# Optimization experiments

Hardware: AMD Instinct MI355X
Metric: run time of the kernel (lower is better)

Reference implementation:

```python
import jax, jax.numpy as jnp
import numpy as np
from jax import lax

NB = 65536          # voxels (seeds) per batch element
C = 256             # feature dim
NUM_CLASS = 3
MAX_NPOINTS = 4096  # per-batch top-k keep
FPS_NPOINTS = 2048  # farthest-point samples
OFFSET_RANGE = np.array([3.0, 3.0, 2.0], dtype=np.float32)
BN_EPS = 1e-5


def _bn_relu(x, gamma, beta):
    # nn.BatchNorm1d in training mode: batch statistics over N
    m = jnp.mean(x, axis=0)
    v = jnp.var(x, axis=0)
    return jax.nn.relu((x - m) * lax.rsqrt(v + BN_EPS) * gamma + beta)


def _vote_mlp(x, w1, g1, b1, w2, b2):
    # Linear(bias=False) -> BN -> ReLU -> Linear(bias)
    return _bn_relu(x @ w1, g1, b1) @ w2 + b2


def _fps(xyz, k):
    # D-FPS (PointNet++ furthest_point_sample): start at index 0,
    # iteratively pick the point with max min-distance to selected set.
    M = xyz.shape[0]

    def step(carry, _):
        dist, last = carry
        d = jnp.sum((xyz - xyz[last]) ** 2, axis=-1)
        dist = jnp.minimum(dist, d)
        nxt = jnp.argmax(dist).astype(jnp.int32)
        return (dist, nxt), nxt

    init = (jnp.full((M,), 1e10, xyz.dtype), jnp.int32(0))
    _, idxs = lax.scan(step, init, None, length=k - 1)
    return jnp.concatenate([jnp.zeros((1,), jnp.int32), idxs])


def setup_inputs() -> dict:
    key = jax.random.key(0)
    ks = jax.random.split(key, 8)
    B = 4
    N = B * NB
    seed_xyz = jax.random.uniform(ks[0], (N, 3), jnp.float32) * jnp.array([70.0, 80.0, 4.0]) - jnp.array([0.0, 40.0, 3.0])
    seed_feats = jax.random.normal(ks[1], (N, C), jnp.float32)
    s = 0.02
    inp = {
        "seed_xyz": seed_xyz,
        "seed_feats": seed_feats,
        "w_off1": jax.random.normal(ks[2], (C, C), jnp.float32) * s,
        "g_off1": jnp.ones((C,), jnp.float32),
        "be_off1": jnp.zeros((C,), jnp.float32),
        "w_off2": jax.random.normal(ks[3], (C, 3), jnp.float32) * s,
        "b_off2": jnp.zeros((3,), jnp.float32),
        "w_cls1": jax.random.normal(ks[4], (C, C), jnp.float32) * s,
        "g_cls1": jnp.ones((C,), jnp.float32),
        "be_cls1": jnp.zeros((C,), jnp.float32),
        "w_cls2": jax.random.normal(ks[5], (C, NUM_CLASS), jnp.float32) * s,
        "b_cls2": jnp.full((NUM_CLASS,), -2.19, jnp.float32),  # cls bias init fill(-2.19)
        "batch_size": B,
    }
    return inp


def reference(seed_xyz, seed_feats, w_off1, g_off1, be_off1, w_off2, b_off2,
              w_cls1, g_cls1, be_cls1, w_cls2, b_cls2, batch_size):
    B = int(batch_size)
    off_rng = jnp.asarray(OFFSET_RANGE)

    # VoteLayer
    seed_offset = _vote_mlp(seed_feats, w_off1, g_off1, be_off1, w_off2, b_off2)   # (N,3)
    seed_cls = _vote_mlp(seed_feats, w_cls1, g_cls1, be_cls1, w_cls2, b_cls2)      # (N,num_class)
    limited = jnp.clip(seed_offset, -off_rng, off_rng)
    votes_xyz = seed_xyz + limited                                                 # (N,3)

    # fps_pool_layer: per-batch topk + D-FPS
    scores = jnp.max(seed_cls, axis=-1)                                            # (N,)
    scores_b = scores.reshape(B, NB)
    xyz_b = seed_xyz.reshape(B, NB, 3)

    def per_batch(sc, xyz):
        _, topk_idx = lax.top_k(jax.nn.sigmoid(sc), MAX_NPOINTS)   # (K,)
        fidx = _fps(xyz[topk_idx], FPS_NPOINTS)                    # (P,) local in topk set
        return topk_idx[fidx]                                      # remap to per-batch index

    local_idx = jax.vmap(per_batch)(scores_b, xyz_b)               # (B, P)
    fps_indices = (local_idx + jnp.arange(B, dtype=local_idx.dtype)[:, None] * NB).reshape(-1)

    bs_col = jnp.repeat(jnp.arange(B, dtype=jnp.float32), NB)[:, None]
    seeds = jnp.concatenate([bs_col, seed_xyz], axis=-1)           # (N,4)
    votes = jnp.concatenate([bs_col, votes_xyz], axis=-1)          # (N,4)

    vote_candidates = lax.stop_gradient(votes[fps_indices])        # .detach() in torch
    vote_features = seed_feats[fps_indices]                        # (B*P, C)

    return (vote_candidates, vote_features, seeds, seed_cls, votes, fps_indices)
```

## Files before the change

kernel.cpp:

```cpp
#include <hip/hip_runtime.h>

#define NB_V 65536
#define TOPK 4096
#define FPSK 2048

typedef short bf16x8 __attribute__((ext_vector_type(8)));
typedef float f32x4 __attribute__((ext_vector_type(4)));

__global__ __launch_bounds__(256, 2) void k_gemm_bf(const float* __restrict__ A,
                                                    const float* __restrict__ W,
                                                    float* __restrict__ H, int N) {
  __shared__ unsigned short As[64][264];
  __shared__ unsigned short Bs[64][264];
  const int tid = threadIdx.x;
  const int cb = blockIdx.x & 3;
  const int rb = blockIdx.x >> 2;
#pragma unroll
  for (int l = 0; l < 16; ++l) {
    int f = tid + 256 * l;
    int r = f >> 6, c4 = (f & 63) << 2;
    float4 v = *reinterpret_cast<const float4*>(&A[(size_t)(rb * 64 + r) * 256 + c4]);
    ushort4 u;
    u.x = (unsigned short)(__float_as_uint(v.x) >> 16);
    u.y = (unsigned short)(__float_as_uint(v.y) >> 16);
    u.z = (unsigned short)(__float_as_uint(v.z) >> 16);
    u.w = (unsigned short)(__float_as_uint(v.w) >> 16);
    *reinterpret_cast<ushort4*>(&As[r][c4]) = u;
  }
  {
    const int c = tid & 63;
    const int kg = tid >> 6;
#pragma unroll
    for (int j = 0; j < 16; ++j) {
      int k0 = kg * 64 + j * 4;
      ushort4 u;
      u.x = (unsigned short)(__float_as_uint(W[(size_t)(k0 + 0) * 256 + cb * 64 + c]) >> 16);
      u.y = (unsigned short)(__float_as_uint(W[(size_t)(k0 + 1) * 256 + cb * 64 + c]) >> 16);
      u.z = (unsigned short)(__float_as_uint(W[(size_t)(k0 + 2) * 256 + cb * 64 + c]) >> 16);
      u.w = (unsigned short)(__float_as_uint(W[(size_t)(k0 + 3) * 256 + cb * 64 + c]) >> 16);
      *reinterpret_cast<ushort4*>(&Bs[c][k0]) = u;
    }
  }
  __syncthreads();
  const int lane = tid & 63, w = tid >> 6;
  const int m = lane & 15, kq = lane >> 4;
  f32x4 acc[4];
#pragma unroll
  for (int s = 0; s < 4; ++s) acc[s] = (f32x4){0.f, 0.f, 0.f, 0.f};
#pragma unroll
  for (int k0 = 0; k0 < 256; k0 += 32) {
    bf16x8 a = *reinterpret_cast<const bf16x8*>(&As[w * 16 + m][k0 + kq * 8]);
#pragma unroll
    for (int s = 0; s < 4; ++s) {
      bf16x8 bfr = *reinterpret_cast<const bf16x8*>(&Bs[s * 16 + m][k0 + kq * 8]);
      acc[s] = __builtin_amdgcn_mfma_f32_16x16x32_bf16(a, bfr, acc[s], 0, 0, 0);
    }
  }
#pragma unroll
  for (int s = 0; s < 4; ++s)
#pragma unroll
    for (int i = 0; i < 4; ++i)
      H[(size_t)(rb * 64 + w * 16 + kq * 4 + i) * 256 + cb * 64 + s * 16 + m] = acc[s][i];
}

__global__ __launch_bounds__(256) void k_gemm64(const float* __restrict__ A,
                                                const float* __restrict__ W,
                                                float* __restrict__ H, int N) {
  __shared__ double Asm[64][33];
  __shared__ double Bsm[32][65];
  const int tid = threadIdx.x;
  const int tx = tid & 15, ty = tid >> 4;
  const int cb = blockIdx.x & 3;
  const int rb = blockIdx.x >> 2;
  double acc[4][4];
#pragma unroll
  for (int i = 0; i < 4; ++i)
#pragma unroll
    for (int j = 0; j < 4; ++j) acc[i][j] = 0.0;

  for (int kc = 0; kc < 256; kc += 32) {
#pragma unroll
    for (int l = 0; l < 8; ++l) {
      int f = tid + 256 * l;
      int r = f >> 5, c = f & 31;
      Asm[r][c] = (double)A[(size_t)(rb * 64 + r) * 256 + kc + c];
    }
#pragma unroll
    for (int l = 0; l < 8; ++l) {
      int f = tid + 256 * l;
      int kr = f >> 6, c = f & 63;
      Bsm[kr][c] = (double)W[(size_t)(kc + kr) * 256 + cb * 64 + c];
    }
    __syncthreads();
#pragma unroll 4
    for (int kk = 0; kk < 32; ++kk) {
      double a0[4], b0[4];
#pragma unroll
      for (int i = 0; i < 4; ++i) a0[i] = Asm[ty + 16 * i][kk];
#pragma unroll
      for (int j = 0; j < 4; ++j) b0[j] = Bsm[kk][tx + 16 * j];
#pragma unroll
      for (int i = 0; i < 4; ++i)
#pragma unroll
        for (int j = 0; j < 4; ++j) acc[i][j] += a0[i] * b0[j];
    }
    __syncthreads();
  }
#pragma unroll
  for (int i = 0; i < 4; ++i)
#pragma unroll
    for (int j = 0; j < 4; ++j)
      H[(size_t)(rb * 64 + ty + 16 * i) * 256 + cb * 64 + tx + 16 * j] = (float)acc[i][j];
}

__global__ __launch_bounds__(256) void k_stats(const float* __restrict__ Hoff,
                                               const float* __restrict__ Hcls,
                                               double* __restrict__ part, int N) {
  const int rpb = N / 1024;
  const int r0 = blockIdx.x * rpb;
  const int t = threadIdx.x;
  double s0 = 0, q0 = 0, s1 = 0, q1 = 0;
  for (int r = r0; r < r0 + rpb; ++r) {
    double v = (double)Hoff[(size_t)r * 256 + t];
    s0 += v; q0 = fma(v, v, q0);
    double w = (double)Hcls[(size_t)r * 256 + t];
    s1 += w; q1 = fma(w, w, q1);
  }
  double* o = part + ((size_t)blockIdx.x * 512 + t) * 2;
  o[0] = s0; o[1] = q0;
  o = part + ((size_t)blockIdx.x * 512 + 256 + t) * 2;
  o[0] = s1; o[1] = q1;
}

__global__ void k_statsfin(const double* __restrict__ part,
                           const float* __restrict__ g_off, const float* __restrict__ be_off,
                           const float* __restrict__ g_cls, const float* __restrict__ be_cls,
                           double* __restrict__ aarr, double* __restrict__ carr,
                           int nparts, int N) {
  const int c = threadIdx.x;
  double s = 0, q = 0;
  for (int p = 0; p < nparts; ++p) {
    s += part[((size_t)p * 512 + c) * 2];
    q += part[((size_t)p * 512 + c) * 2 + 1];
  }
  double mean = s / (double)N;
  double var = q / (double)N - mean * mean;
  double g = (c < 256) ? (double)g_off[c] : (double)g_cls[c - 256];
  double be = (c < 256) ? (double)be_off[c] : (double)be_cls[c - 256];
  double a = g / sqrt(var + 1e-5);
  aarr[c] = a;
  carr[c] = be - mean * a;
}

__global__ __launch_bounds__(256) void k_fuse(const float* __restrict__ Hoff,
                                              const float* __restrict__ Hcls,
                                              const float* __restrict__ xyz,
                                              const float* __restrict__ w_off2,
                                              const float* __restrict__ b_off2,
                                              const float* __restrict__ w_cls2,
                                              const float* __restrict__ b_cls2,
                                              const double* __restrict__ aarr,
                                              const double* __restrict__ carr,
                                              float* __restrict__ out_seeds,
                                              float* __restrict__ out_cls,
                                              float* __restrict__ out_votes,
                                              unsigned long long* __restrict__ keys,
                                              int N) {
  __shared__ double sa[512], sc[512];
  __shared__ double w2[512][3];
  const int tid = threadIdx.x;
  for (int i = tid; i < 512; i += 256) {
    sa[i] = aarr[i];
    sc[i] = carr[i];
#pragma unroll
    for (int k = 0; k < 3; ++k)
      w2[i][k] = (i < 256) ? (double)w_off2[i * 3 + k] : (double)w_cls2[(i - 256) * 3 + k];
  }
  __syncthreads();
  const int lane = tid & 63, wid = tid >> 6;
  const int gw = blockIdx.x * 4 + wid;
  for (int r = gw; r < N; r += 4096) {
    double po0 = 0, po1 = 0, po2 = 0, pc0 = 0, pc1 = 0, pc2 = 0;
#pragma unroll
    for (int q = 0; q < 4; ++q) {
      int c = lane + 64 * q;
      double h = (double)Hoff[(size_t)r * 256 + c];
      double v = fma(h, sa[c], sc[c]);
      v = v > 0.0 ? v : 0.0;
      po0 = fma(v, w2[c][0], po0);
      po1 = fma(v, w2[c][1], po1);
      po2 = fma(v, w2[c][2], po2);
      int c2 = 256 + c;
      double h2 = (double)Hcls[(size_t)r * 256 + c];
      double v2 = fma(h2, sa[c2], sc[c2]);
      v2 = v2 > 0.0 ? v2 : 0.0;
      pc0 = fma(v2, w2[c2][0], pc0);
      pc1 = fma(v2, w2[c2][1], pc1);
      pc2 = fma(v2, w2[c2][2], pc2);
    }
#pragma unroll
    for (int off = 32; off; off >>= 1) {
      po0 += __shfl_xor(po0, off); po1 += __shfl_xor(po1, off); po2 += __shfl_xor(po2, off);
      pc0 += __shfl_xor(pc0, off); pc1 += __shfl_xor(pc1, off); pc2 += __shfl_xor(pc2, off);
    }
    if (lane == 0) {
      float x = xyz[(size_t)r * 3], y = xyz[(size_t)r * 3 + 1], z = xyz[(size_t)r * 3 + 2];
      float bs = (float)(r >> 16);
      out_seeds[(size_t)r * 4 + 0] = bs;
      out_seeds[(size_t)r * 4 + 1] = x;
      out_seeds[(size_t)r * 4 + 2] = y;
      out_seeds[(size_t)r * 4 + 3] = z;
      double offv[3] = {po0 + (double)b_off2[0], po1 + (double)b_off2[1], po2 + (double)b_off2[2]};
      const double rng[3] = {3.0, 3.0, 2.0};
      float pxyz[3] = {x, y, z};
      out_votes[(size_t)r * 4 + 0] = bs;
#pragma unroll
      for (int k = 0; k < 3; ++k) {
        double lim = offv[k];
        lim = lim < -rng[k] ? -rng[k] : lim;
        lim = lim > rng[k] ? rng[k] : lim;
        out_votes[(size_t)r * 4 + 1 + k] = (float)((double)pxyz[k] + lim);
      }
      double c0 = pc0 + (double)b_cls2[0];
      double c1 = pc1 + (double)b_cls2[1];
      double c2v = pc2 + (double)b_cls2[2];
      out_cls[(size_t)r * 3 + 0] = (float)c0;
      out_cls[(size_t)r * 3 + 1] = (float)c1;
      out_cls[(size_t)r * 3 + 2] = (float)c2v;
      double s = c0 > c1 ? c0 : c1;
      s = s > c2v ? s : c2v;
      long long bits = __double_as_longlong(s);
      unsigned long long key =
          bits >= 0 ? ((unsigned long long)bits | 0x8000000000000000ull) : ~((unsigned long long)bits);
      keys[r] = key;
    }
  }
}

__global__ __launch_bounds__(1024) void k_topk(const unsigned long long* __restrict__ keys,
                                               unsigned int* __restrict__ topk) {
  const int b = blockIdx.x;
  const unsigned long long* K = keys + (size_t)b * NB_V;
  __shared__ unsigned int hist[256];
  __shared__ unsigned long long pfx_s;
  __shared__ int want_s;
  __shared__ unsigned long long skey[TOPK];
  __shared__ unsigned int sidx[TOPK];
  __shared__ int cnt_hi, cnt_eq;
  __shared__ unsigned int eq_idx[1024];
  const int tid = threadIdx.x;
  if (tid == 0) { pfx_s = 0ull; want_s = TOPK; }
  __syncthreads();
  for (int p = 0; p < 8; ++p) {
    const int shift = 56 - 8 * p;
    if (tid < 256) hist[tid] = 0;
    __syncthreads();
    unsigned long long pfx = pfx_s;
    for (int i = tid; i < NB_V; i += 1024) {
      unsigned long long k = K[i];
      bool ok;
      if (p == 0) ok = true;
      else ok = ((k >> (shift + 8)) == (pfx >> (shift + 8)));
      if (ok) atomicAdd(&hist[(unsigned)(k >> shift) & 255u], 1u);
    }
    __syncthreads();
    if (tid == 0) {
      int want = want_s;
      int cum = 0, d = 255;
      for (; d >= 0; --d) {
        int c = (int)hist[d];
        if (cum + c >= want) break;
        cum += c;
      }
      want_s = want - cum;
      pfx_s = pfx_s | ((unsigned long long)d << shift);
    }
    __syncthreads();
  }
  const unsigned long long Kthr = pfx_s;
  const int T = want_s;
  if (tid == 0) { cnt_hi = 0; cnt_eq = 0; }
  __syncthreads();
  for (int i = tid; i < NB_V; i += 1024) {
    unsigned long long k = K[i];
    if (k > Kthr) {
      int pos = atomicAdd(&cnt_hi, 1);
      skey[pos] = k;
      sidx[pos] = (unsigned)i;
    } else if (k == Kthr) {
      int pos = atomicAdd(&cnt_eq, 1);
      if (pos < 1024) eq_idx[pos] = (unsigned)i;
    }
  }
  __syncthreads();
  if (tid == 0) {
    int m = cnt_eq; if (m > 1024) m = 1024;
    for (int a2 = 1; a2 < m; ++a2) {
      unsigned v = eq_idx[a2];
      int b2 = a2 - 1;
      while (b2 >= 0 && eq_idx[b2] > v) { eq_idx[b2 + 1] = eq_idx[b2]; --b2; }
      eq_idx[b2 + 1] = v;
    }
    for (int t = 0; t < T; ++t) { skey[cnt_hi + t] = Kthr; sidx[cnt_hi + t] = eq_idx[t]; }
  }
  __syncthreads();
  for (int k2 = 2; k2 <= TOPK; k2 <<= 1) {
    for (int j = k2 >> 1; j > 0; j >>= 1) {
      for (int i = tid; i < TOPK; i += 1024) {
        int ix = i ^ j;
        if (ix > i) {
          unsigned long long ka = skey[i], kb = skey[ix];
          unsigned int ia = sidx[i], ib = sidx[ix];
          bool a_first = (ka > kb) || (ka == kb && ia < ib);
          bool up = (i & k2) == 0;
          if (up ? !a_first : a_first) {
            skey[i] = kb; skey[ix] = ka;
            sidx[i] = ib; sidx[ix] = ia;
          }
        }
      }
      __syncthreads();
    }
  }
  for (int i = tid; i < TOPK; i += 1024) topk[(size_t)b * TOPK + i] = sidx[i];
}

template <int CTRL>
__device__ __forceinline__ void dpp_merge2(unsigned long long& v, int& p) {
  unsigned lo = (unsigned)v, hi = (unsigned)(v >> 32);
  unsigned olo = (unsigned)__builtin_amdgcn_update_dpp(0, (int)lo, CTRL, 0xF, 0xF, false);
  unsigned ohi = (unsigned)__builtin_amdgcn_update_dpp(0, (int)hi, CTRL, 0xF, 0xF, false);
  int op = __builtin_amdgcn_update_dpp(0, p, CTRL, 0xF, 0xF, false);
  unsigned long long ov = ((unsigned long long)ohi << 32) | (unsigned long long)olo;
  bool t = (ov > v) || (ov == v && op < p);
  v = t ? ov : v;
  p = t ? op : p;
}

__device__ __forceinline__ void shfl_merge2(unsigned long long& v, int& p, int mask) {
  unsigned long long ov = __shfl_xor(v, mask);
  int op = __shfl_xor(p, mask);
  bool t = (ov > v) || (ov == v && op < p);
  v = t ? ov : v;
  p = t ? op : p;
}

#define FPS_REP16(M) M(0) M(1) M(2) M(3) M(4) M(5) M(6) M(7) \
                     M(8) M(9) M(10) M(11) M(12) M(13) M(14) M(15)

__global__ __launch_bounds__(256, 1) void k_fps(const float* __restrict__ xyz,
                                                const unsigned int* __restrict__ topk,
                                                unsigned int* __restrict__ fpspos) {
  const int b = blockIdx.x;
  const int tid = threadIdx.x;
  __shared__ float4 cpos[TOPK];
  __shared__ ulonglong2 wv[2][4];
  __shared__ float4 wc[2][4];

#define FPS_DECL(J) float x##J, y##J, z##J; double d##J;
  FPS_REP16(FPS_DECL)

#define FPS_INIT(J) { \
    int p = tid + 256 * (J); \
    unsigned idx = topk[(size_t)b * TOPK + p]; \
    size_t base = ((size_t)b * NB_V + idx) * 3; \
    x##J = xyz[base]; y##J = xyz[base + 1]; z##J = xyz[base + 2]; \
    d##J = 1e10; \
    cpos[p] = make_float4(x##J, y##J, z##J, 0.0f); }
  FPS_REP16(FPS_INIT)

  if (tid == 0) {
    wc[0][0] = make_float4(x0, y0, z0, 0.0f);
    fpspos[(size_t)b * FPSK] = 0u;
  }
  __syncthreads();
  float4 s0 = wc[0][0];
  float sx = s0.x, sy = s0.y, sz = s0.z;
  const int lane = tid & 63, wid = tid >> 6;

  for (int it = 1; it < FPSK; ++it) {
    const int par = it & 1;
    double lx = (double)sx, ly = (double)sy, lz = (double)sz;
    unsigned long long cv0, cv1;
    int cp0, cp1;
#define FPS_UPD(J) { \
    double dx = (double)x##J - lx; \
    double dy = (double)y##J - ly; \
    double dz = (double)z##J - lz; \
    double dd = __dadd_rn(__dadd_rn(__dmul_rn(dx, dx), __dmul_rn(dy, dy)), __dmul_rn(dz, dz)); \
    d##J = fmin(d##J, dd); \
    unsigned long long db = (unsigned long long)__double_as_longlong(d##J); \
    if ((J) == 0) { cv0 = db; cp0 = tid; } \
    else if ((J) == 1) { cv1 = db; cp1 = tid + 256; } \
    else if (((J) & 1) == 0) { bool g = db > cv0; cv0 = g ? db : cv0; cp0 = g ? (tid + 256 * (J)) : cp0; } \
    else { bool g = db > cv1; cv1 = g ? db : cv1; cp1 = g ? (tid + 256 * (J)) : cp1; } }
    FPS_REP16(FPS_UPD)
    {
      bool g = (cv1 > cv0) || (cv1 == cv0 && cp1 < cp0);
      cv0 = g ? cv1 : cv0;
      cp0 = g ? cp1 : cp0;
    }
    dpp_merge2<0xB1>(cv0, cp0);
    dpp_merge2<0x4E>(cv0, cp0);
    dpp_merge2<0x124>(cv0, cp0);
    dpp_merge2<0x128>(cv0, cp0);
    shfl_merge2(cv0, cp0, 16);
    shfl_merge2(cv0, cp0, 32);
    float4 wpos = cpos[cp0];
    if (lane == 0) {
      wv[par][wid] = make_ulonglong2(cv0, (unsigned long long)(unsigned)cp0);
      wc[par][wid] = wpos;
    }
    __syncthreads();
    ulonglong2 e0 = wv[par][0];
    float4 q0 = wc[par][0];
    unsigned long long bv = e0.x;
    int bp = (int)e0.y;
    float fx = q0.x, fy = q0.y, fz = q0.z;
#pragma unroll
    for (int w = 1; w < 4; ++w) {
      ulonglong2 e = wv[par][w];
      float4 q = wc[par][w];
      bool t = (e.x > bv) || (e.x == bv && (int)e.y < bp);
      bv = t ? e.x : bv;
      bp = t ? (int)e.y : bp;
      fx = t ? q.x : fx;
      fy = t ? q.y : fy;
      fz = t ? q.z : fz;
    }
    sx = fx; sy = fy; sz = fz;
    if (tid == 0) fpspos[(size_t)b * FPSK + it] = (unsigned)bp;
  }
}

__global__ __launch_bounds__(256) void k_gather(const unsigned int* __restrict__ topk,
                                                const unsigned int* __restrict__ fpspos,
                                                const float* __restrict__ feats,
                                                const float* __restrict__ votes_out,
                                                float* __restrict__ o0, float* __restrict__ o1,
                                                float* __restrict__ o5) {
  const int r = blockIdx.x;
  const int b = r / FPSK;
  __shared__ unsigned int gsh;
  if (threadIdx.x == 0) {
    unsigned pos = fpspos[r];
    unsigned local = topk[(size_t)b * TOPK + pos];
    gsh = (unsigned)(b * NB_V) + local;
  }
  __syncthreads();
  const unsigned g = gsh;
  o1[(size_t)r * 256 + threadIdx.x] = feats[(size_t)g * 256 + threadIdx.x];
  if (threadIdx.x < 4) o0[(size_t)r * 4 + threadIdx.x] = votes_out[(size_t)g * 4 + threadIdx.x];
  if (threadIdx.x == 4) o5[r] = (float)g;
}

extern "C" void kernel_launch(void* const* d_in, const int* in_sizes, int n_in,
                              void* d_out, int out_size, void* d_ws, size_t ws_size,
                              hipStream_t stream) {
  const float* xyz = (const float*)d_in[0];
  const float* feats = (const float*)d_in[1];
  const float* w_off1 = (const float*)d_in[2];
  const float* g_off1 = (const float*)d_in[3];
  const float* be_off1 = (const float*)d_in[4];
  const float* w_off2 = (const float*)d_in[5];
  const float* b_off2 = (const float*)d_in[6];
  const float* w_cls1 = (const float*)d_in[7];
  const float* g_cls1 = (const float*)d_in[8];
  const float* be_cls1 = (const float*)d_in[9];
  const float* w_cls2 = (const float*)d_in[10];
  const float* b_cls2 = (const float*)d_in[11];

  const int N = in_sizes[0] / 3;
  const int B = N / NB_V;
  const int BP = B * FPSK;

  float* out = (float*)d_out;
  float* o0 = out;
  float* o1 = o0 + (size_t)BP * 4;
  float* o2 = o1 + (size_t)BP * 256;
  float* o3 = o2 + (size_t)N * 4;
  float* o4 = o3 + (size_t)N * 3;
  float* o5 = o4 + (size_t)N * 4;

  char* w = (char*)d_ws;
  float* Hoff = (float*)w;
  float* Hcls = (float*)(w + (size_t)N * 1024);
  double* part = (double*)(w + (size_t)N * 2048);
  double* aarr = (double*)(w + (size_t)N * 2048 + 8388608);
  double* carr = aarr + 512;
  unsigned long long* keys =
      (unsigned long long*)(w + (size_t)N * 2048 + 8388608 + 8192);
  unsigned int* topkbuf = (unsigned int*)((char*)keys + (size_t)N * 8);
  unsigned int* fpspos = topkbuf + (size_t)B * TOPK;

  k_gemm_bf<<<dim3((N / 64) * 4), dim3(256), 0, stream>>>(feats, w_off1, Hoff, N);
  k_gemm64<<<dim3((N / 64) * 4), dim3(256), 0, stream>>>(feats, w_cls1, Hcls, N);
  k_stats<<<dim3(1024), dim3(256), 0, stream>>>(Hoff, Hcls, part, N);
  k_statsfin<<<dim3(1), dim3(512), 0, stream>>>(part, g_off1, be_off1, g_cls1, be_cls1,
                                                aarr, carr, 1024, N);
  k_fuse<<<dim3(1024), dim3(256), 0, stream>>>(Hoff, Hcls, xyz, w_off2, b_off2, w_cls2,
                                               b_cls2, aarr, carr, o2, o3, o4, keys, N);
  k_topk<<<dim3(B), dim3(1024), 0, stream>>>(keys, topkbuf);
  k_fps<<<dim3(B), dim3(256), 0, stream>>>(xyz, topkbuf, fpspos);
  k_gather<<<dim3(BP), dim3(256), 0, stream>>>(topkbuf, fpspos, feats, o4, o0, o1, o5);
}
```

Measured before the change: 4.160 ms.

## Overlap serial FPS with offset-branch GEMM by reordering pipeline and fusing kernels

```diff
diff --git a/kernel.cpp b/kernel.cpp
--- a/kernel.cpp
+++ b/kernel.cpp
@@ -6,62 +6,6 @@
 
 typedef short bf16x8 __attribute__((ext_vector_type(8)));
 typedef float f32x4 __attribute__((ext_vector_type(4)));
-
-__global__ __launch_bounds__(256, 2) void k_gemm_bf(const float* __restrict__ A,
-                                                    const float* __restrict__ W,
-                                                    float* __restrict__ H, int N) {
-  __shared__ unsigned short As[64][264];
-  __shared__ unsigned short Bs[64][264];
-  const int tid = threadIdx.x;
-  const int cb = blockIdx.x & 3;
-  const int rb = blockIdx.x >> 2;
-#pragma unroll
-  for (int l = 0; l < 16; ++l) {
-    int f = tid + 256 * l;
-    int r = f >> 6, c4 = (f & 63) << 2;
-    float4 v = *reinterpret_cast<const float4*>(&A[(size_t)(rb * 64 + r) * 256 + c4]);
-    ushort4 u;
-    u.x = (unsigned short)(__float_as_uint(v.x) >> 16);
-    u.y = (unsigned short)(__float_as_uint(v.y) >> 16);
-    u.z = (unsigned short)(__float_as_uint(v.z) >> 16);
-    u.w = (unsigned short)(__float_as_uint(v.w) >> 16);
-    *reinterpret_cast<ushort4*>(&As[r][c4]) = u;
-  }
-  {
-    const int c = tid & 63;
-    const int kg = tid >> 6;
-#pragma unroll
-    for (int j = 0; j < 16; ++j) {
-      int k0 = kg * 64 + j * 4;
-      ushort4 u;
-      u.x = (unsigned short)(__float_as_uint(W[(size_t)(k0 + 0) * 256 + cb * 64 + c]) >> 16);
-      u.y = (unsigned short)(__float_as_uint(W[(size_t)(k0 + 1) * 256 + cb * 64 + c]) >> 16);
-      u.z = (unsigned short)(__float_as_uint(W[(size_t)(k0 + 2) * 256 + cb * 64 + c]) >> 16);
-      u.w = (unsigned short)(__float_as_uint(W[(size_t)(k0 + 3) * 256 + cb * 64 + c]) >> 16);
-      *reinterpret_cast<ushort4*>(&Bs[c][k0]) = u;
-    }
-  }
-  __syncthreads();
-  const int lane = tid & 63, w = tid >> 6;
-  const int m = lane & 15, kq = lane >> 4;
-  f32x4 acc[4];
-#pragma unroll
-  for (int s = 0; s < 4; ++s) acc[s] = (f32x4){0.f, 0.f, 0.f, 0.f};
-#pragma unroll
-  for (int k0 = 0; k0 < 256; k0 += 32) {
-    bf16x8 a = *reinterpret_cast<const bf16x8*>(&As[w * 16 + m][k0 + kq * 8]);
-#pragma unroll
-    for (int s = 0; s < 4; ++s) {
-      bf16x8 bfr = *reinterpret_cast<const bf16x8*>(&Bs[s * 16 + m][k0 + kq * 8]);
-      acc[s] = __builtin_amdgcn_mfma_f32_16x16x32_bf16(a, bfr, acc[s], 0, 0, 0);
-    }
-  }
-#pragma unroll
-  for (int s = 0; s < 4; ++s)
-#pragma unroll
-    for (int i = 0; i < 4; ++i)
-      H[(size_t)(rb * 64 + w * 16 + kq * 4 + i) * 256 + cb * 64 + s * 16 + m] = acc[s][i];
-}
 
 __global__ __launch_bounds__(256) void k_gemm64(const float* __restrict__ A,
                                                 const float* __restrict__ W,
@@ -113,95 +57,78 @@
       H[(size_t)(rb * 64 + ty + 16 * i) * 256 + cb * 64 + tx + 16 * j] = (float)acc[i][j];
 }
 
-__global__ __launch_bounds__(256) void k_stats(const float* __restrict__ Hoff,
-                                               const float* __restrict__ Hcls,
-                                               double* __restrict__ part, int N) {
+__global__ __launch_bounds__(256) void k_stats1(const float* __restrict__ H,
+                                                double* __restrict__ part, int N) {
   const int rpb = N / 1024;
   const int r0 = blockIdx.x * rpb;
   const int t = threadIdx.x;
-  double s0 = 0, q0 = 0, s1 = 0, q1 = 0;
+  double s = 0, q = 0;
   for (int r = r0; r < r0 + rpb; ++r) {
-    double v = (double)Hoff[(size_t)r * 256 + t];
-    s0 += v; q0 = fma(v, v, q0);
-    double w = (double)Hcls[(size_t)r * 256 + t];
-    s1 += w; q1 = fma(w, w, q1);
-  }
-  double* o = part + ((size_t)blockIdx.x * 512 + t) * 2;
-  o[0] = s0; o[1] = q0;
-  o = part + ((size_t)blockIdx.x * 512 + 256 + t) * 2;
-  o[0] = s1; o[1] = q1;
-}
-
-__global__ void k_statsfin(const double* __restrict__ part,
-                           const float* __restrict__ g_off, const float* __restrict__ be_off,
-                           const float* __restrict__ g_cls, const float* __restrict__ be_cls,
-                           double* __restrict__ aarr, double* __restrict__ carr,
-                           int nparts, int N) {
+    double v = (double)H[(size_t)r * 256 + t];
+    s += v;
+    q = fma(v, v, q);
+  }
+  double* o = part + ((size_t)blockIdx.x * 256 + t) * 2;
+  o[0] = s;
+  o[1] = q;
+}
+
+__global__ void k_statsfin1(const double* __restrict__ part,
+                            const float* __restrict__ gam, const float* __restrict__ bet,
+                            double* __restrict__ aarr, double* __restrict__ carr,
+                            int nparts, int N) {
   const int c = threadIdx.x;
   double s = 0, q = 0;
   for (int p = 0; p < nparts; ++p) {
-    s += part[((size_t)p * 512 + c) * 2];
-    q += part[((size_t)p * 512 + c) * 2 + 1];
+    s += part[((size_t)p * 256 + c) * 2];
+    q += part[((size_t)p * 256 + c) * 2 + 1];
   }
   double mean = s / (double)N;
   double var = q / (double)N - mean * mean;
-  double g = (c < 256) ? (double)g_off[c] : (double)g_cls[c - 256];
-  double be = (c < 256) ? (double)be_off[c] : (double)be_cls[c - 256];
-  double a = g / sqrt(var + 1e-5);
+  double a = (double)gam[c] / sqrt(var + 1e-5);
   aarr[c] = a;
-  carr[c] = be - mean * a;
-}
-
-__global__ __launch_bounds__(256) void k_fuse(const float* __restrict__ Hoff,
-                                              const float* __restrict__ Hcls,
-                                              const float* __restrict__ xyz,
-                                              const float* __restrict__ w_off2,
-                                              const float* __restrict__ b_off2,
-                                              const float* __restrict__ w_cls2,
-                                              const float* __restrict__ b_cls2,
-                                              const double* __restrict__ aarr,
-                                              const double* __restrict__ carr,
-                                              float* __restrict__ out_seeds,
-                                              float* __restrict__ out_cls,
-                                              float* __restrict__ out_votes,
-                                              unsigned long long* __restrict__ keys,
-                                              int N) {
-  __shared__ double sa[512], sc[512];
-  __shared__ double w2[512][3];
+  carr[c] = (double)bet[c] - mean * a;
+}
+
+__global__ __launch_bounds__(256) void k_fuse_cls(const float* __restrict__ Hcls,
+                                                  const float* __restrict__ xyz,
+                                                  const float* __restrict__ w_cls2,
+                                                  const float* __restrict__ b_cls2,
+                                                  const double* __restrict__ aarr,
+                                                  const double* __restrict__ carr,
+                                                  float* __restrict__ out_seeds,
+                                                  float* __restrict__ out_cls,
+                                                  unsigned long long* __restrict__ keys,
+                                                  int N) {
+  __shared__ double sa[256], sc[256];
+  __shared__ double w2[256][3];
   const int tid = threadIdx.x;
-  for (int i = tid; i < 512; i += 256) {
-    sa[i] = aarr[i];
-    sc[i] = carr[i];
-#pragma unroll
-    for (int k = 0; k < 3; ++k)
-      w2[i][k] = (i < 256) ? (double)w_off2[i * 3 + k] : (double)w_cls2[(i - 256) * 3 + k];
+  {
+    sa[tid] = aarr[tid];
+    sc[tid] = carr[tid];
+#pragma unroll
+    for (int k = 0; k < 3; ++k) w2[tid][k] = (double)w_cls2[tid * 3 + k];
   }
   __syncthreads();
   const int lane = tid & 63, wid = tid >> 6;
   const int gw = blockIdx.x * 4 + wid;
   for (int r = gw; r < N; r += 4096) {
-    double po0 = 0, po1 = 0, po2 = 0, pc0 = 0, pc1 = 0, pc2 = 0;
+    double pc0 = 0, pc1 = 0, pc2 = 0;
 #pragma unroll
     for (int q = 0; q < 4; ++q) {
       int c = lane + 64 * q;
-      double h = (double)Hoff[(size_t)r * 256 + c];
-      double v = fma(h, sa[c], sc[c]);
-      v = v > 0.0 ? v : 0.0;
-      po0 = fma(v, w2[c][0], po0);
-      po1 = fma(v, w2[c][1], po1);
-      po2 = fma(v, w2[c][2], po2);
-      int c2 = 256 + c;
       double h2 = (double)Hcls[(size_t)r * 256 + c];
-      double v2 = fma(h2, sa[c2], sc[c2]);
+      double v2 = fma(h2, sa[c], sc[c]);
       v2 = v2 > 0.0 ? v2 : 0.0;
-      pc0 = fma(v2, w2[c2][0], pc0);
-      pc1 = fma(v2, w2[c2][1], pc1);
-      pc2 = fma(v2, w2[c2][2], pc2);
+      pc0 = fma(v2, w2[c][0], pc0);
+      pc1 = fma(v2, w2[c][1], pc1);
+      pc2 = fma(v2, w2[c][2], pc2);
     }
 #pragma unroll
     for (int off = 32; off; off >>= 1) {
-      po0 += __shfl_xor(po0, off); po1 += __shfl_xor(po1, off); po2 += __shfl_xor(po2, off);
-      pc0 += __shfl_xor(pc0, off); pc1 += __shfl_xor(pc1, off); pc2 += __shfl_xor(pc2, off);
+      pc0 += __shfl_xor(pc0, off);
+      pc1 += __shfl_xor(pc1, off);
+      pc2 += __shfl_xor(pc2, off);
     }
     if (lane == 0) {
       float x = xyz[(size_t)r * 3], y = xyz[(size_t)r * 3 + 1], z = xyz[(size_t)r * 3 + 2];
@@ -210,17 +137,6 @@
       out_seeds[(size_t)r * 4 + 1] = x;
       out_seeds[(size_t)r * 4 + 2] = y;
       out_seeds[(size_t)r * 4 + 3] = z;
-      double offv[3] = {po0 + (double)b_off2[0], po1 + (double)b_off2[1], po2 + (double)b_off2[2]};
-      const double rng[3] = {3.0, 3.0, 2.0};
-      float pxyz[3] = {x, y, z};
-      out_votes[(size_t)r * 4 + 0] = bs;
-#pragma unroll
-      for (int k = 0; k < 3; ++k) {
-        double lim = offv[k];
-        lim = lim < -rng[k] ? -rng[k] : lim;
-        lim = lim > rng[k] ? rng[k] : lim;
-        out_votes[(size_t)r * 4 + 1 + k] = (float)((double)pxyz[k] + lim);
-      }
       double c0 = pc0 + (double)b_cls2[0];
       double c1 = pc1 + (double)b_cls2[1];
       double c2v = pc2 + (double)b_cls2[2];
@@ -233,6 +149,62 @@
       unsigned long long key =
           bits >= 0 ? ((unsigned long long)bits | 0x8000000000000000ull) : ~((unsigned long long)bits);
       keys[r] = key;
+    }
+  }
+}
+
+__global__ __launch_bounds__(256) void k_fuse_off(const float* __restrict__ Hoff,
+                                                  const float* __restrict__ xyz,
+                                                  const float* __restrict__ w_off2,
+                                                  const float* __restrict__ b_off2,
+                                                  const double* __restrict__ aarr,
+                                                  const double* __restrict__ carr,
+                                                  float* __restrict__ out_votes,
+                                                  int N) {
+  __shared__ double sa[256], sc[256];
+  __shared__ double w2[256][3];
+  const int tid = threadIdx.x;
+  {
+    sa[tid] = aarr[tid];
+    sc[tid] = carr[tid];
+#pragma unroll
+    for (int k = 0; k < 3; ++k) w2[tid][k] = (double)w_off2[tid * 3 + k];
+  }
+  __syncthreads();
+  const int lane = tid & 63, wid = tid >> 6;
+  const int gw = blockIdx.x * 4 + wid;
+  for (int r = gw; r < N; r += 4096) {
+    double po0 = 0, po1 = 0, po2 = 0;
+#pragma unroll
+    for (int q = 0; q < 4; ++q) {
+      int c = lane + 64 * q;
+      double h = (double)Hoff[(size_t)r * 256 + c];
+      double v = fma(h, sa[c], sc[c]);
+      v = v > 0.0 ? v : 0.0;
+      po0 = fma(v, w2[c][0], po0);
+      po1 = fma(v, w2[c][1], po1);
+      po2 = fma(v, w2[c][2], po2);
+    }
+#pragma unroll
+    for (int off = 32; off; off >>= 1) {
+      po0 += __shfl_xor(po0, off);
+      po1 += __shfl_xor(po1, off);
+      po2 += __shfl_xor(po2, off);
+    }
+    if (lane == 0) {
+      float x = xyz[(size_t)r * 3], y = xyz[(size_t)r * 3 + 1], z = xyz[(size_t)r * 3 + 2];
+      float bs = (float)(r >> 16);
+      double offv[3] = {po0 + (double)b_off2[0], po1 + (double)b_off2[1], po2 + (double)b_off2[2]};
+      const double rng[3] = {3.0, 3.0, 2.0};
+      float pxyz[3] = {x, y, z};
+      out_votes[(size_t)r * 4 + 0] = bs;
+#pragma unroll
+      for (int k = 0; k < 3; ++k) {
+        double lim = offv[k];
+        lim = lim < -rng[k] ? -rng[k] : lim;
+        lim = lim > rng[k] ? rng[k] : lim;
+        out_votes[(size_t)r * 4 + 1 + k] = (float)((double)pxyz[k] + lim);
+      }
     }
   }
 }
@@ -337,28 +309,32 @@
   p = t ? op : p;
 }
 
-__device__ __forceinline__ void shfl_merge2(unsigned long long& v, int& p, int mask) {
-  unsigned long long ov = __shfl_xor(v, mask);
-  int op = __shfl_xor(p, mask);
-  bool t = (ov > v) || (ov == v && op < p);
-  v = t ? ov : v;
-  p = t ? op : p;
+__device__ __forceinline__ unsigned long long rdlane64(unsigned long long v, int l) {
+  unsigned lo = (unsigned)__builtin_amdgcn_readlane((int)(unsigned)v, l);
+  unsigned hi = (unsigned)__builtin_amdgcn_readlane((int)(unsigned)(v >> 32), l);
+  return ((unsigned long long)hi << 32) | (unsigned long long)lo;
 }
 
 #define FPS_REP16(M) M(0) M(1) M(2) M(3) M(4) M(5) M(6) M(7) \
                      M(8) M(9) M(10) M(11) M(12) M(13) M(14) M(15)
 
-__global__ __launch_bounds__(256, 1) void k_fps(const float* __restrict__ xyz,
-                                                const unsigned int* __restrict__ topk,
-                                                unsigned int* __restrict__ fpspos) {
-  const int b = blockIdx.x;
+__global__ __launch_bounds__(256, 2) void k_fused(const float* __restrict__ xyz,
+                                                  const unsigned int* __restrict__ topk,
+                                                  unsigned int* __restrict__ fpspos,
+                                                  const float* __restrict__ A,
+                                                  const float* __restrict__ W,
+                                                  float* __restrict__ H, int N) {
+  __shared__ __align__(16) char smem[67584];
   const int tid = threadIdx.x;
-  __shared__ float4 cpos[TOPK];
-  __shared__ ulonglong2 wv[2][4];
-  __shared__ float4 wc[2][4];
+
+  if (blockIdx.x < 4) {
+    float4* cpos = (float4*)smem;
+    ulonglong2(*wv)[4] = (ulonglong2(*)[4])(smem + 65536);
+    float4(*wc)[4] = (float4(*)[4])(smem + 65792);
+    const int b = blockIdx.x;
 
 #define FPS_DECL(J) float x##J, y##J, z##J; double d##J;
-  FPS_REP16(FPS_DECL)
+    FPS_REP16(FPS_DECL)
 
 #define FPS_INIT(J) { \
     int p = tid + 256 * (J); \
@@ -367,22 +343,22 @@
     x##J = xyz[base]; y##J = xyz[base + 1]; z##J = xyz[base + 2]; \
     d##J = 1e10; \
     cpos[p] = make_float4(x##J, y##J, z##J, 0.0f); }
-  FPS_REP16(FPS_INIT)
-
-  if (tid == 0) {
-    wc[0][0] = make_float4(x0, y0, z0, 0.0f);
-    fpspos[(size_t)b * FPSK] = 0u;
-  }
-  __syncthreads();
-  float4 s0 = wc[0][0];
-  float sx = s0.x, sy = s0.y, sz = s0.z;
-  const int lane = tid & 63, wid = tid >> 6;
-
-  for (int it = 1; it < FPSK; ++it) {
-    const int par = it & 1;
-    double lx = (double)sx, ly = (double)sy, lz = (double)sz;
-    unsigned long long cv0, cv1;
-    int cp0, cp1;
+    FPS_REP16(FPS_INIT)
+
+    if (tid == 0) {
+      wc[0][0] = make_float4(x0, y0, z0, 0.0f);
+      fpspos[(size_t)b * FPSK] = 0u;
+    }
+    __syncthreads();
+    float4 s0 = wc[0][0];
+    float sx = s0.x, sy = s0.y, sz = s0.z;
+    const int lane = tid & 63, wid = tid >> 6;
+
+    for (int it = 1; it < FPSK; ++it) {
+      const int par = it & 1;
+      double lx = (double)sx, ly = (double)sy, lz = (double)sz;
+      unsigned long long cv0, cv1;
+      int cp0, cp1;
 #define FPS_UPD(J) { \
     double dx = (double)x##J - lx; \
     double dy = (double)y##J - ly; \
@@ -394,42 +370,102 @@
     else if ((J) == 1) { cv1 = db; cp1 = tid + 256; } \
     else if (((J) & 1) == 0) { bool g = db > cv0; cv0 = g ? db : cv0; cp0 = g ? (tid + 256 * (J)) : cp0; } \
     else { bool g = db > cv1; cv1 = g ? db : cv1; cp1 = g ? (tid + 256 * (J)) : cp1; } }
-    FPS_REP16(FPS_UPD)
+      FPS_REP16(FPS_UPD)
+      {
+        bool g = (cv1 > cv0) || (cv1 == cv0 && cp1 < cp0);
+        cv0 = g ? cv1 : cv0;
+        cp0 = g ? cp1 : cp0;
+      }
+      dpp_merge2<0xB1>(cv0, cp0);
+      dpp_merge2<0x4E>(cv0, cp0);
+      dpp_merge2<0x124>(cv0, cp0);
+      dpp_merge2<0x128>(cv0, cp0);
+      unsigned long long r0v = rdlane64(cv0, 0), r1v = rdlane64(cv0, 16);
+      unsigned long long r2v = rdlane64(cv0, 32), r3v = rdlane64(cv0, 48);
+      int r0p = __builtin_amdgcn_readlane(cp0, 0);
+      int r1p = __builtin_amdgcn_readlane(cp0, 16);
+      int r2p = __builtin_amdgcn_readlane(cp0, 32);
+      int r3p = __builtin_amdgcn_readlane(cp0, 48);
+      if ((r1v > r0v) || (r1v == r0v && r1p < r0p)) { r0v = r1v; r0p = r1p; }
+      if ((r2v > r0v) || (r2v == r0v && r2p < r0p)) { r0v = r2v; r0p = r2p; }
+      if ((r3v > r0v) || (r3v == r0v && r3p < r0p)) { r0v = r3v; r0p = r3p; }
+      float4 wpos = cpos[r0p];
+      if (lane == 0) {
+        wv[par][wid] = make_ulonglong2(r0v, (unsigned long long)(unsigned)r0p);
+        wc[par][wid] = wpos;
+      }
+      __syncthreads();
+      ulonglong2 e0 = wv[par][0];
+      float4 q0 = wc[par][0];
+      unsigned long long bv = e0.x;
+      int bp = (int)e0.y;
+      float fx = q0.x, fy = q0.y, fz = q0.z;
+#pragma unroll
+      for (int w = 1; w < 4; ++w) {
+        ulonglong2 e = wv[par][w];
+        float4 q = wc[par][w];
+        bool t = (e.x > bv) || (e.x == bv && (int)e.y < bp);
+        bv = t ? e.x : bv;
+        bp = t ? (int)e.y : bp;
+        fx = t ? q.x : fx;
+        fy = t ? q.y : fy;
+        fz = t ? q.z : fz;
+      }
+      sx = fx; sy = fy; sz = fz;
+      if (tid == 0) fpspos[(size_t)b * FPSK + it] = (unsigned)bp;
+    }
+  } else {
+    unsigned short(*As)[264] = (unsigned short(*)[264])smem;
+    unsigned short(*Bs)[264] = (unsigned short(*)[264])(smem + 33792);
+    const int gb = blockIdx.x - 4;
+    const int cb = gb & 3;
+    const int rb = gb >> 2;
+#pragma unroll
+    for (int l = 0; l < 16; ++l) {
+      int f = tid + 256 * l;
+      int r = f >> 6, c4 = (f & 63) << 2;
+      float4 v = *reinterpret_cast<const float4*>(&A[(size_t)(rb * 64 + r) * 256 + c4]);
+      ushort4 u;
+      u.x = (unsigned short)(__float_as_uint(v.x) >> 16);
+      u.y = (unsigned short)(__float_as_uint(v.y) >> 16);
+      u.z = (unsigned short)(__float_as_uint(v.z) >> 16);
+      u.w = (unsigned short)(__float_as_uint(v.w) >> 16);
+      *reinterpret_cast<ushort4*>(&As[r][c4]) = u;
+    }
     {
-      bool g = (cv1 > cv0) || (cv1 == cv0 && cp1 < cp0);
-      cv0 = g ? cv1 : cv0;
-      cp0 = g ? cp1 : cp0;
-    }
-    dpp_merge2<0xB1>(cv0, cp0);
-    dpp_merge2<0x4E>(cv0, cp0);
-    dpp_merge2<0x124>(cv0, cp0);
-    dpp_merge2<0x128>(cv0, cp0);
-    shfl_merge2(cv0, cp0, 16);
-    shfl_merge2(cv0, cp0, 32);
-    float4 wpos = cpos[cp0];
-    if (lane == 0) {
-      wv[par][wid] = make_ulonglong2(cv0, (unsigned long long)(unsigned)cp0);
-      wc[par][wid] = wpos;
-    }
-    __syncthreads();
-    ulonglong2 e0 = wv[par][0];
-    float4 q0 = wc[par][0];
-    unsigned long long bv = e0.x;
-    int bp = (int)e0.y;
-    float fx = q0.x, fy = q0.y, fz = q0.z;
-#pragma unroll
-    for (int w = 1; w < 4; ++w) {
-      ulonglong2 e = wv[par][w];
-      float4 q = wc[par][w];
-      bool t = (e.x > bv) || (e.x == bv && (int)e.y < bp);
-      bv = t ? e.x : bv;
-      bp = t ? (int)e.y : bp;
-      fx = t ? q.x : fx;
-      fy = t ? q.y : fy;
-      fz = t ? q.z : fz;
-    }
-    sx = fx; sy = fy; sz = fz;
-    if (tid == 0) fpspos[(size_t)b * FPSK + it] = (unsigned)bp;
+      const int c = tid & 63;
+      const int kg = tid >> 6;
+#pragma unroll
+      for (int j = 0; j < 16; ++j) {
+        int k0 = kg * 64 + j * 4;
+        ushort4 u;
+        u.x = (unsigned short)(__float_as_uint(W[(size_t)(k0 + 0) * 256 + cb * 64 + c]) >> 16);
+        u.y = (unsigned short)(__float_as_uint(W[(size_t)(k0 + 1) * 256 + cb * 64 + c]) >> 16);
+        u.z = (unsigned short)(__float_as_uint(W[(size_t)(k0 + 2) * 256 + cb * 64 + c]) >> 16);
+        u.w = (unsigned short)(__float_as_uint(W[(size_t)(k0 + 3) * 256 + cb * 64 + c]) >> 16);
+        *reinterpret_cast<ushort4*>(&Bs[c][k0]) = u;
+      }
+    }
+    __syncthreads();
+    const int lane = tid & 63, w = tid >> 6;
+    const int m = lane & 15, kq = lane >> 4;
+    f32x4 acc[4];
+#pragma unroll
+    for (int s = 0; s < 4; ++s) acc[s] = (f32x4){0.f, 0.f, 0.f, 0.f};
+#pragma unroll
+    for (int k0 = 0; k0 < 256; k0 += 32) {
+      bf16x8 a = *reinterpret_cast<const bf16x8*>(&As[w * 16 + m][k0 + kq * 8]);
+#pragma unroll
+      for (int s = 0; s < 4; ++s) {
+        bf16x8 bfr = *reinterpret_cast<const bf16x8*>(&Bs[s * 16 + m][k0 + kq * 8]);
+        acc[s] = __builtin_amdgcn_mfma_f32_16x16x32_bf16(a, bfr, acc[s], 0, 0, 0);
+      }
+    }
+#pragma unroll
+    for (int s = 0; s < 4; ++s)
+#pragma unroll
+      for (int i = 0; i < 4; ++i)
+        H[(size_t)(rb * 64 + w * 16 + kq * 4 + i) * 256 + cb * 64 + s * 16 + m] = acc[s][i];
   }
 }
 
@@ -485,22 +521,27 @@
   char* w = (char*)d_ws;
   float* Hoff = (float*)w;
   float* Hcls = (float*)(w + (size_t)N * 1024);
-  double* part = (double*)(w + (size_t)N * 2048);
-  double* aarr = (double*)(w + (size_t)N * 2048 + 8388608);
-  double* carr = aarr + 512;
-  unsigned long long* keys =
-      (unsigned long long*)(w + (size_t)N * 2048 + 8388608 + 8192);
+  char* p0 = w + (size_t)N * 2048;
+  double* part_cls = (double*)p0;
+  double* part_off = (double*)(p0 + 4194304);
+  double* a_cls = (double*)(p0 + 8388608);
+  double* c_cls = a_cls + 256;
+  double* a_off = c_cls + 256;
+  double* c_off = a_off + 256;
+  unsigned long long* keys = (unsigned long long*)(p0 + 8388608 + 8192);
   unsigned int* topkbuf = (unsigned int*)((char*)keys + (size_t)N * 8);
   unsigned int* fpspos = topkbuf + (size_t)B * TOPK;
 
-  k_gemm_bf<<<dim3((N / 64) * 4), dim3(256), 0, stream>>>(feats, w_off1, Hoff, N);
   k_gemm64<<<dim3((N / 64) * 4), dim3(256), 0, stream>>>(feats, w_cls1, Hcls, N);
-  k_stats<<<dim3(1024), dim3(256), 0, stream>>>(Hoff, Hcls, part, N);
-  k_statsfin<<<dim3(1), dim3(512), 0, stream>>>(part, g_off1, be_off1, g_cls1, be_cls1,
-                                                aarr, carr, 1024, N);
-  k_fuse<<<dim3(1024), dim3(256), 0, stream>>>(Hoff, Hcls, xyz, w_off2, b_off2, w_cls2,
-                                               b_cls2, aarr, carr, o2, o3, o4, keys, N);
+  k_stats1<<<dim3(1024), dim3(256), 0, stream>>>(Hcls, part_cls, N);
+  k_statsfin1<<<dim3(1), dim3(256), 0, stream>>>(part_cls, g_cls1, be_cls1, a_cls, c_cls, 1024, N);
+  k_fuse_cls<<<dim3(1024), dim3(256), 0, stream>>>(Hcls, xyz, w_cls2, b_cls2, a_cls, c_cls,
+                                                   o2, o3, keys, N);
   k_topk<<<dim3(B), dim3(1024), 0, stream>>>(keys, topkbuf);
-  k_fps<<<dim3(B), dim3(256), 0, stream>>>(xyz, topkbuf, fpspos);
+  k_fused<<<dim3(4 + (N / 64) * 4), dim3(256), 0, stream>>>(xyz, topkbuf, fpspos,
+                                                            feats, w_off1, Hoff, N);
+  k_stats1<<<dim3(1024), dim3(256), 0, stream>>>(Hoff, part_off, N);
+  k_statsfin1<<<dim3(1), dim3(256), 0, stream>>>(part_off, g_off1, be_off1, a_off, c_off, 1024, N);
+  k_fuse_off<<<dim3(1024), dim3(256), 0, stream>>>(Hoff, xyz, w_off2, b_off2, a_off, c_off, o4, N);
   k_gather<<<dim3(BP), dim3(256), 0, stream>>>(topkbuf, fpspos, feats, o4, o0, o1, o5);
 }
```

Result: slower. 4.423 ms (+6.3%).
